# Kernel tuning notes

Measured on AMD Instinct MI355X. Metric: run time of the kernel, lower is better.

## Reference

```python
import jax, jax.numpy as jnp
import numpy as np

N_EMBD = 768
N_HEAD = 8
HEAD_DIM = N_EMBD // N_HEAD


def setup_inputs() -> dict:
    key = jax.random.key(0)
    k1, k2, k3, k4, k5 = jax.random.split(key, 5)
    B, T, C = 8, 1024, N_EMBD
    scale = 0.02
    return {
        "x": jax.random.normal(k1, (B, T, C), dtype=jnp.float32),
        "W_attn": jax.random.normal(k2, (C, 3 * C), dtype=jnp.float32) * scale,
        "b_attn": jnp.zeros((3 * C,), dtype=jnp.float32),
        "W_proj": jax.random.normal(k3, (C, C), dtype=jnp.float32) * scale,
        "b_proj": jnp.zeros((C,), dtype=jnp.float32),
    }


def reference(x, W_attn, b_attn, W_proj, b_proj):
    B, T, C = x.shape
    H, D = N_HEAD, HEAD_DIM
    qkv = x @ W_attn + b_attn                      # [B,T,3C]
    q, k, v = jnp.split(qkv, 3, axis=-1)
    # [B,H,T,D]
    q = q.reshape(B, T, H, D).transpose(0, 2, 1, 3)
    k = k.reshape(B, T, H, D).transpose(0, 2, 1, 3)
    v = v.reshape(B, T, H, D).transpose(0, 2, 1, 3)
    att = jnp.einsum("bhqd,bhkd->bhqk", q, k) * (1.0 / jnp.sqrt(jnp.float32(D)))
    causal = jnp.tril(jnp.ones((T, T), dtype=bool))
    att = jnp.where(causal[None, None], att, jnp.float32(-jnp.inf))
    att = jax.nn.softmax(att, axis=-1)
    y = jnp.einsum("bhqk,bhkd->bhqd", att, v)      # [B,H,T,D]
    y = y.transpose(0, 2, 1, 3).reshape(B, T, C)
    return y @ W_proj + b_proj
```

## Files before the change

kernel.cpp:

```cpp
#include <hip/hip_runtime.h>
#include <math.h>

#define B_ 8
#define T_ 1024
#define C_ 768
#define H_ 8
#define D_ 96
#define M_ (B_ * T_)
#define N1_ (3 * C_)
#define KD_ 768

typedef __bf16 bf16x8 __attribute__((ext_vector_type(8)));
typedef float f32x4 __attribute__((ext_vector_type(4)));
typedef float f32x16 __attribute__((ext_vector_type(16)));

__device__ __forceinline__ unsigned short f2bf(float f) {
  unsigned int u = __float_as_uint(f);
  u += 0x7FFF + ((u >> 16) & 1);
  return (unsigned short)(u >> 16);
}

__device__ __forceinline__ void load_lds16(const void* g, void* l) {
  __builtin_amdgcn_global_load_lds(
      (const __attribute__((address_space(1))) unsigned int*)g,
      (__attribute__((address_space(3))) unsigned int*)l, 16, 0, 0);
}

__global__ __launch_bounds__(256) void prep_kernel(
    const float* __restrict__ x, unsigned short* __restrict__ xb,
    const float* __restrict__ Wa, unsigned short* __restrict__ WaT,
    const float* __restrict__ Wp, unsigned short* __restrict__ WpT) {
  __shared__ float Lt[32][33];
  int bid = blockIdx.x;
  if (bid < 6144) {
    int i = (bid * 256 + threadIdx.x) * 4;
    float4 v = *(const float4*)(x + i);
    ushort4 o;
    o.x = f2bf(v.x); o.y = f2bf(v.y); o.z = f2bf(v.z); o.w = f2bf(v.w);
    *(ushort4*)(xb + i) = o;
    return;
  }
  bid -= 6144;
  const float* W; unsigned short* WT; int Nd;
  if (bid < 1728) { W = Wa; WT = WaT; Nd = N1_; }
  else            { W = Wp; WT = WpT; Nd = C_; bid -= 1728; }
  const int r0 = (bid % 24) * 32;
  const int c0 = (bid / 24) * 32;
#pragma unroll
  for (int i = 0; i < 4; ++i) {
    int e = threadIdx.x + 256 * i;
    int r = e >> 5, c = e & 31;
    Lt[r][c] = W[(size_t)(r0 + r) * Nd + c0 + c];
  }
  __syncthreads();
#pragma unroll
  for (int i = 0; i < 4; ++i) {
    int e = threadIdx.x + 256 * i;
    int rr = e >> 5, cc = e & 31;
    WT[(size_t)(c0 + rr) * KD_ + r0 + cc] = f2bf(Lt[cc][rr]);
  }
}

__global__ __launch_bounds__(512, 2) void gemm256_kernel(
    const unsigned short* __restrict__ A, const unsigned short* __restrict__ Bt,
    const float* __restrict__ bias, unsigned short* __restrict__ Cout,
    unsigned short* __restrict__ vt, float sc) {
  __shared__ __align__(16) unsigned short Sb[2][64 * 512];
  const int tid = threadIdx.x;
  const int w = tid >> 6, l = tid & 63;
  const int l31 = l & 31, lh = l >> 5;
  const int wm = w >> 2, wn = w & 3;

  const int bid = blockIdx.x;
  const int xcd = bid & 7, j = bid >> 3;
  const int m0 = (xcd * 4 + (j & 3)) * 256;
  const int n0 = (j >> 2) * 256;

  f32x16 acc[4][2];
#pragma unroll
  for (int mi = 0; mi < 4; ++mi)
#pragma unroll
    for (int ni = 0; ni < 2; ++ni)
#pragma unroll
      for (int r = 0; r < 16; ++r) acc[mi][ni][r] = 0.f;

  const unsigned short* gbase[2];
  int cb_[2];
#pragma unroll
  for (int i = 0; i < 2; ++i) {
    const int u = w * 2 + i;
    if (u < 8) {
      gbase[i] = A + (size_t)(m0 + u * 32 + l31) * KD_ + lh * 8;
      cb_[i] = u * 4;
    } else {
      gbase[i] = Bt + (size_t)(n0 + (u - 8) * 32 + l31) * KD_ + lh * 8;
      cb_[i] = 32 + (u - 8) * 4;
    }
  }
  auto stage_unit = [&](int g) {
    const int buf = (g >> 2) & 1, kh = g & 3;
#pragma unroll
    for (int i = 0; i < 2; ++i)
      load_lds16(gbase[i] + g * 16, &Sb[buf][(cb_[i] + kh) * 512]);
  };

#pragma unroll
  for (int g = 0; g < 7; ++g) stage_unit(g);
  asm volatile("s_waitcnt vmcnt(6)" ::: "memory");
  __builtin_amdgcn_s_barrier();
  asm volatile("" ::: "memory");

  for (int it = 0; it < 6; ++it) {
#pragma unroll
    for (int p = 0; p < 8; ++p) {
      const int buf = p >> 2;
      const int kh = p & 3;
      bf16x8 af[4], bfr[2];
#pragma unroll
      for (int mi = 0; mi < 4; ++mi)
        af[mi] = *(const bf16x8*)&Sb[buf][((wm * 4 + mi) * 4 + kh) * 512 + l * 8];
#pragma unroll
      for (int ni = 0; ni < 2; ++ni)
        bfr[ni] = *(const bf16x8*)&Sb[buf][(32 + (wn * 2 + ni) * 4 + kh) * 512 + l * 8];
      const int g = 8 * it + 7 + p;
      if (g < 48) stage_unit(g);
      asm volatile("" ::: "memory");
      __builtin_amdgcn_s_barrier();
      asm volatile("" ::: "memory");
      __builtin_amdgcn_s_setprio(1);
#pragma unroll
      for (int mi = 0; mi < 4; ++mi)
#pragma unroll
        for (int ni = 0; ni < 2; ++ni)
          acc[mi][ni] = __builtin_amdgcn_mfma_f32_32x32x16_bf16(
              af[mi], bfr[ni], acc[mi][ni], 0, 0, 0);
      __builtin_amdgcn_s_setprio(0);
      if (p == 3) {
        if (it == 5) asm volatile("s_waitcnt vmcnt(0)" ::: "memory");
        else         asm volatile("s_waitcnt vmcnt(6)" ::: "memory");
      } else if (p == 7 && it < 5) {
        asm volatile("s_waitcnt vmcnt(6)" ::: "memory");
      }
      asm volatile("" ::: "memory");
      __builtin_amdgcn_s_barrier();
      asm volatile("" ::: "memory");
    }
  }

#pragma unroll
  for (int mi = 0; mi < 4; ++mi) {
    const int rowb = m0 + wm * 128 + mi * 32 + 4 * lh;
#pragma unroll
    for (int ni = 0; ni < 2; ++ni) {
      const int col = n0 + wn * 64 + ni * 32 + l31;
      const float bv = bias[col];
      if (col < 1536) {
        const float mul = (col < C_) ? sc : 1.f;
#pragma unroll
        for (int r = 0; r < 16; ++r) {
          const int row = rowb + (r & 3) + 8 * (r >> 2);
          Cout[(size_t)row * N1_ + col] = f2bf((acc[mi][ni][r] + bv) * mul);
        }
      } else {
        const int x = col - 1536;
        const int h = x / 96, d = x % 96;
#pragma unroll
        for (int r = 0; r < 16; ++r) {
          const int row = rowb + (r & 3) + 8 * (r >> 2);
          const int bb = row >> 10, t = row & 1023;
          vt[((size_t)(bb * H_ + h) * D_ + d) * T_ + t] =
              f2bf(acc[mi][ni][r] + bv);
        }
      }
    }
  }
}

template <int WM32, bool OUTF32, bool VSCAT>
__global__ __launch_bounds__(256, WM32 == 2 ? 3 : 4) void gemm_mfma_kernel(
    const unsigned short* __restrict__ A, const unsigned short* __restrict__ Bt,
    const float* __restrict__ bias, void* __restrict__ Cout,
    unsigned short* __restrict__ vt, int N,
    int sc_lim, float sc, int mmask, int mshift) {
  constexpr int AS2 = 2 * WM32;
  constexpr int NCH = AS2 * 2 + 8;
  constexpr int CPW = NCH / 4;
  __shared__ __align__(16) unsigned short Sb[3][NCH * 512];
  const int tid = threadIdx.x;
  const int w = tid >> 6, l = tid & 63;
  const int l31 = l & 31, lh = l >> 5;
  const int bid = blockIdx.x;
  const int m0 = (bid & mmask) * (AS2 * 32), n0 = (bid >> mshift) * 128;
  const int wrb = (w >> 1) * WM32;
  const int wnb = (w & 1) * 2;

  f32x16 acc[WM32][2];
#pragma unroll
  for (int i = 0; i < WM32; ++i)
#pragma unroll
    for (int j = 0; j < 2; ++j)
#pragma unroll
      for (int r = 0; r < 16; ++r) acc[i][j][r] = 0.f;

  const unsigned short* gp[CPW];
#pragma unroll
  for (int i = 0; i < CPW; ++i) {
    const int c = w * CPW + i;
    const int pr = c >> 1, kh = c & 1;
    gp[i] = (pr < AS2)
        ? A  + (size_t)(m0 + pr * 32 + l31) * KD_ + kh * 16 + lh * 8
        : Bt + (size_t)(n0 + (pr - AS2) * 32 + l31) * KD_ + kh * 16 + lh * 8;
  }

#pragma unroll
  for (int t = 0; t < 2; ++t)
#pragma unroll
    for (int i = 0; i < CPW; ++i) {
      load_lds16(gp[i], &Sb[t][(w * CPW + i) * 512]);
      gp[i] += 32;
    }

  int cur = 0, stg = 2;
  for (int k0 = 0; k0 < KD_; k0 += 32) {
    if (k0 + 32 < KD_) {
      if constexpr (CPW == 4) asm volatile("s_waitcnt vmcnt(4)" ::: "memory");
      else                    asm volatile("s_waitcnt vmcnt(3)" ::: "memory");
    } else {
      asm volatile("s_waitcnt vmcnt(0)" ::: "memory");
    }
    __builtin_amdgcn_s_barrier();
    asm volatile("" ::: "memory");

    if (k0 + 64 < KD_) {
#pragma unroll
      for (int i = 0; i < CPW; ++i) {
        load_lds16(gp[i], &Sb[stg][(w * CPW + i) * 512]);
        gp[i] += 32;
      }
    }

#pragma unroll
    for (int kh = 0; kh < 2; ++kh) {
      bf16x8 af[WM32], bfr[2];
#pragma unroll
      for (int mi = 0; mi < WM32; ++mi)
        af[mi] = *(const bf16x8*)&Sb[cur][((wrb + mi) * 2 + kh) * 512 + l * 8];
#pragma unroll
      for (int ni = 0; ni < 2; ++ni)
        bfr[ni] = *(const bf16x8*)&Sb[cur][((AS2 + wnb + ni) * 2 + kh) * 512 + l * 8];
#pragma unroll
      for (int mi = 0; mi < WM32; ++mi)
#pragma unroll
        for (int ni = 0; ni < 2; ++ni)
          acc[mi][ni] = __builtin_amdgcn_mfma_f32_32x32x16_bf16(
              af[mi], bfr[ni], acc[mi][ni], 0, 0, 0);
    }
    cur = (cur == 2) ? 0 : cur + 1;
    stg = (stg == 2) ? 0 : stg + 1;
  }

  const bool vblock = VSCAT && (n0 >= 1536);
#pragma unroll
  for (int mi = 0; mi < WM32; ++mi) {
    const int rowb = m0 + (wrb + mi) * 32 + 4 * lh;
#pragma unroll
    for (int ni = 0; ni < 2; ++ni) {
      const int col = n0 + (wnb + ni) * 32 + l31;
      const float bv = bias[col];
      if (!vblock) {
        const float mul = (col < sc_lim) ? sc : 1.f;
#pragma unroll
        for (int r = 0; r < 16; ++r) {
          const int row = rowb + (r & 3) + 8 * (r >> 2);
          float v = (acc[mi][ni][r] + bv) * mul;
          if (OUTF32)
            ((float*)Cout)[(size_t)row * N + col] = v;
          else
            ((unsigned short*)Cout)[(size_t)row * N + col] = f2bf(v);
        }
      } else {
        const int x = col - 1536;
        const int h = x / 96, d = x % 96;
#pragma unroll
        for (int r = 0; r < 16; ++r) {
          const int row = rowb + (r & 3) + 8 * (r >> 2);
          const int bb = row >> 10, t = row & 1023;
          vt[((size_t)(bb * H_ + h) * D_ + d) * T_ + t] =
              f2bf(acc[mi][ni][r] + bv);
        }
      }
    }
  }
}

__global__ __launch_bounds__(256) void attn_mfma_kernel(
    const unsigned short* __restrict__ qkv,
    const unsigned short* __restrict__ vt,
    unsigned short* __restrict__ y) {
  __shared__ __align__(16) unsigned short KV[2][24 * 512];
  __shared__ __align__(16) unsigned short Pt[4][16][72];

  const int tid = threadIdx.x;
  const int w = tid >> 6, l = tid & 63;
  const int lm = l & 15, lq = l >> 4;
  const int bh = blockIdx.x & 63, pi = blockIdx.x >> 6;
  const int b = bh >> 3, h = bh & 7;
  const size_t bT = (size_t)b * T_;

  bf16x8 onef;
#pragma unroll
  for (int i = 0; i < 8; ++i) onef[i] = (__bf16)1.0f;

  auto issue = [&](int j0, int buf) {
#pragma unroll
    for (int i = 0; i < 6; ++i) {
      const int c = w * 6 + i;
      const unsigned short* g;
      if (c < 12) {
        const int kc = c >> 2, nb = c & 3;
        g = qkv + (bT + j0 + nb * 16 + lm) * N1_ + C_ + h * D_ + kc * 32 + lq * 8;
      } else {
        const int cv = c - 12;
        const int db = cv >> 1, vc = cv & 1;
        g = vt + ((size_t)bh * D_ + db * 16 + lm) * T_ + j0 + vc * 32 + lq * 8;
      }
      load_lds16(g, &KV[buf][c * 512]);
    }
  };

  int cur = 0;
  issue(0, 0);

  for (int half = 0; half < 2; ++half) {
    const int qt = half ? (15 - pi) : pi;
    const int q0 = qt * 64;

    bf16x8 qf[3];
    {
      const unsigned short* qp =
          qkv + (bT + q0 + w * 16 + lm) * N1_ + h * D_ + lq * 8;
      qf[0] = *(const bf16x8*)(qp);
      qf[1] = *(const bf16x8*)(qp + 32);
      qf[2] = *(const bf16x8*)(qp + 64);
    }
    f32x4 o[7];
#pragma unroll
    for (int i = 0; i < 7; ++i) o[i] = (f32x4){0.f, 0.f, 0.f, 0.f};

    for (int jt = 0; jt <= qt; ++jt) {
      __syncthreads();
      if (jt < qt)          issue((jt + 1) * 64, cur ^ 1);
      else if (half == 0)   issue(0, cur ^ 1);

      const bool diag = (jt == qt);
#pragma unroll
      for (int nb = 0; nb < 4; ++nb) {
        if (diag && nb > w) {
#pragma unroll
          for (int r = 0; r < 4; ++r)
            Pt[w][lq * 4 + r][nb * 16 + lm] = 0;
          continue;
        }
        f32x4 a = (f32x4){0.f, 0.f, 0.f, 0.f};
#pragma unroll
        for (int kc = 0; kc < 3; ++kc) {
          bf16x8 kf = *(const bf16x8*)&KV[cur][(kc * 4 + nb) * 512 + l * 8];
          a = __builtin_amdgcn_mfma_f32_16x16x32_bf16(qf[kc], kf, a, 0, 0, 0);
        }
#pragma unroll
        for (int r = 0; r < 4; ++r) {
          float s = a[r];
          if (diag && (nb * 16 + lm > w * 16 + lq * 4 + r)) s = -INFINITY;
          Pt[w][lq * 4 + r][nb * 16 + lm] = f2bf(__expf(s));
        }
      }

      bf16x8 pf0 = *(const bf16x8*)&Pt[w][lm][lq * 8];
      bf16x8 pf1 = *(const bf16x8*)&Pt[w][lm][32 + lq * 8];
#pragma unroll
      for (int db = 0; db < 6; ++db) {
        bf16x8 vf0 = *(const bf16x8*)&KV[cur][(12 + db * 2 + 0) * 512 + l * 8];
        bf16x8 vf1 = *(const bf16x8*)&KV[cur][(12 + db * 2 + 1) * 512 + l * 8];
        o[db] = __builtin_amdgcn_mfma_f32_16x16x32_bf16(pf0, vf0, o[db], 0, 0, 0);
        o[db] = __builtin_amdgcn_mfma_f32_16x16x32_bf16(pf1, vf1, o[db], 0, 0, 0);
      }
      o[6] = __builtin_amdgcn_mfma_f32_16x16x32_bf16(pf0, onef, o[6], 0, 0, 0);
      o[6] = __builtin_amdgcn_mfma_f32_16x16x32_bf16(pf1, onef, o[6], 0, 0, 0);
      cur ^= 1;
    }

#pragma unroll
    for (int r = 0; r < 4; ++r) {
      const float inv = 1.f / o[6][r];
      const size_t row = bT + q0 + w * 16 + lq * 4 + r;
#pragma unroll
      for (int db = 0; db < 6; ++db)
        y[row * C_ + h * D_ + db * 16 + lm] = f2bf(o[db][r] * inv);
    }
  }
}

extern "C" void kernel_launch(void* const* d_in, const int* in_sizes, int n_in,
                              void* d_out, int out_size, void* d_ws, size_t ws_size,
                              hipStream_t stream) {
  const float* x      = (const float*)d_in[0];
  const float* W_attn = (const float*)d_in[1];
  const float* b_attn = (const float*)d_in[2];
  const float* W_proj = (const float*)d_in[3];
  const float* b_proj = (const float*)d_in[4];
  float* out = (float*)d_out;

  char* ws = (char*)d_ws;
  unsigned short* xb  = (unsigned short*)(ws);
  unsigned short* WaT = (unsigned short*)(ws + 12582912);
  unsigned short* WpT = (unsigned short*)(ws + 16121856);
  unsigned short* qkv = (unsigned short*)(ws + 17301504);
  unsigned short* vt  = (unsigned short*)(ws + 55050240);
  unsigned short* yb  = (unsigned short*)(ws + 67633152);

  const float qscale = 0.10206207261596577f;

  prep_kernel<<<6144 + 2304, 256, 0, stream>>>(x, xb, W_attn, WaT, W_proj, WpT);

  gemm256_kernel<<<(M_ / 256) * (N1_ / 256), 512, 0, stream>>>(
      xb, WaT, b_attn, qkv, vt, qscale);
  attn_mfma_kernel<<<8 * B_ * H_, 256, 0, stream>>>(qkv, vt, yb);
  gemm_mfma_kernel<1, true, false><<<(C_ / 128) * (M_ / 64), 256, 0, stream>>>(
      yb, WpT, b_proj, out, nullptr, C_, 0, 1.f, 127, 7);
}
```

Measured before the change: 224.5 us.

## Restructure GEMM LDS staging into a 9-slot ring with XOR-swizzled layout

Replaces the double-buffered K-split LDS layout of the QKV GEMM with a 9-slot ring buffer. Each slot holds a 128-row by 64-k tile of A or B, loaded with an XOR swizzle on the k offset to avoid bank conflicts. The prefetch depth and waitcnt schedule change to match: four slots are consumed per 64-wide k step while the next tiles stream in. The aim is fewer LDS bank conflicts and more contiguous global loads, at the cost of more LDS (144 KB) and more complex slot indexing.

```diff
diff --git a/kernel.cpp b/kernel.cpp
--- a/kernel.cpp
+++ b/kernel.cpp
@@ -65,7 +65,7 @@
     const unsigned short* __restrict__ A, const unsigned short* __restrict__ Bt,
     const float* __restrict__ bias, unsigned short* __restrict__ Cout,
     unsigned short* __restrict__ vt, float sc) {
-  __shared__ __align__(16) unsigned short Sb[2][64 * 512];
+  __shared__ __align__(16) unsigned short Sb[9 * 8192];
   const int tid = threadIdx.x;
   const int w = tid >> 6, l = tid & 63;
   const int l31 = l & 31, lh = l >> 5;
@@ -84,46 +84,53 @@
 #pragma unroll
       for (int r = 0; r < 16; ++r) acc[mi][ni][r] = 0.f;
 
-  const unsigned short* gbase[2];
-  int cb_[2];
-#pragma unroll
-  for (int i = 0; i < 2; ++i) {
-    const int u = w * 2 + i;
-    if (u < 8) {
-      gbase[i] = A + (size_t)(m0 + u * 32 + l31) * KD_ + lh * 8;
-      cb_[i] = u * 4;
-    } else {
-      gbase[i] = Bt + (size_t)(n0 + (u - 8) * 32 + l31) * KD_ + lh * 8;
-      cb_[i] = 32 + (u - 8) * 4;
-    }
-  }
-  auto stage_unit = [&](int g) {
-    const int buf = (g >> 2) & 1, kh = g & 3;
+  const int srow = 16 * w + (l >> 3);
+  const int skoff = 8 * ((l & 7) ^ (l >> 3));
+  const unsigned short* puA0 = A  + (size_t)(m0 + srow) * KD_ + skoff;
+  const unsigned short* puA1 = A  + (size_t)(m0 + 128 + srow) * KD_ + skoff;
+  const unsigned short* puB0 = Bt + (size_t)(n0 + srow) * KD_ + skoff;
+  const unsigned short* puB1 = Bt + (size_t)(n0 + 128 + srow) * KD_ + skoff;
+
+  auto stage_unit = [&](int g, int slot) {
+    const int u = g & 3, Tg = g >> 2;
+    const unsigned short* base =
+        (u == 0) ? puA0 : (u == 1) ? puA1 : (u == 2) ? puB0 : puB1;
+    const unsigned short* p0 = base + Tg * 64;
 #pragma unroll
     for (int i = 0; i < 2; ++i)
-      load_lds16(gbase[i] + g * 16, &Sb[buf][(cb_[i] + kh) * 512]);
+      load_lds16(p0 + (size_t)i * (8 * KD_),
+                 &Sb[slot * 8192 + w * 1024 + i * 512 + l * 8]);
   };
 
 #pragma unroll
-  for (int g = 0; g < 7; ++g) stage_unit(g);
-  asm volatile("s_waitcnt vmcnt(6)" ::: "memory");
+  for (int g = 0; g < 5; ++g) stage_unit(g, g);
+  asm volatile("s_waitcnt vmcnt(2)" ::: "memory");
   __builtin_amdgcn_s_barrier();
   asm volatile("" ::: "memory");
 
-  for (int it = 0; it < 6; ++it) {
-#pragma unroll
-    for (int p = 0; p < 8; ++p) {
-      const int buf = p >> 2;
-      const int kh = p & 3;
+  int sA = wm;
+  int sB = 2 + (wn >> 1);
+  int sg = 5;
+
+  for (int T = 0; T < 12; ++T) {
+#pragma unroll
+    for (int q = 0; q < 4; ++q) {
+      const int kterm = 8 * ((2 * q + lh) ^ (l31 & 7));
       bf16x8 af[4], bfr[2];
 #pragma unroll
       for (int mi = 0; mi < 4; ++mi)
-        af[mi] = *(const bf16x8*)&Sb[buf][((wm * 4 + mi) * 4 + kh) * 512 + l * 8];
+        af[mi] = *(const bf16x8*)&Sb[sA * 8192 + (mi * 32 + l31) * 64 + kterm];
 #pragma unroll
       for (int ni = 0; ni < 2; ++ni)
-        bfr[ni] = *(const bf16x8*)&Sb[buf][(32 + (wn * 2 + ni) * 4 + kh) * 512 + l * 8];
-      const int g = 8 * it + 7 + p;
-      if (g < 48) stage_unit(g);
+        bfr[ni] = *(const bf16x8*)&Sb[sB * 8192 +
+                                      ((wn & 1) * 64 + ni * 32 + l31) * 64 + kterm];
+      {
+        const int g = 4 * T + q + 5;
+        if (g < 48) {
+          stage_unit(g, sg);
+          sg = (sg == 8) ? 0 : sg + 1;
+        }
+      }
       asm volatile("" ::: "memory");
       __builtin_amdgcn_s_barrier();
       asm volatile("" ::: "memory");
@@ -135,16 +142,16 @@
           acc[mi][ni] = __builtin_amdgcn_mfma_f32_32x32x16_bf16(
               af[mi], bfr[ni], acc[mi][ni], 0, 0, 0);
       __builtin_amdgcn_s_setprio(0);
-      if (p == 3) {
-        if (it == 5) asm volatile("s_waitcnt vmcnt(0)" ::: "memory");
-        else         asm volatile("s_waitcnt vmcnt(6)" ::: "memory");
-      } else if (p == 7 && it < 5) {
-        asm volatile("s_waitcnt vmcnt(6)" ::: "memory");
+      if (q == 3 && T < 11) {
+        if (T == 10) asm volatile("s_waitcnt vmcnt(0)" ::: "memory");
+        else         asm volatile("s_waitcnt vmcnt(2)" ::: "memory");
       }
       asm volatile("" ::: "memory");
       __builtin_amdgcn_s_barrier();
       asm volatile("" ::: "memory");
     }
+    sA += 4; if (sA >= 9) sA -= 9;
+    sB += 4; if (sB >= 9) sB -= 9;
   }
 
 #pragma unroll
```

Result: faster. 213.7 us (-4.8%).
